# Optimization experiments

Measured on AMD Instinct MI355X. Metric: run time of the kernel, lower is better.

Reference implementation:

```python
import jax, jax.numpy as jnp
import numpy as np

B, SQ, SK, D_MODEL, H, D = 2, 2048, 2048, 1024, 16, 64


def setup_inputs() -> dict:
    key = jax.random.key(0)
    ks = jax.random.split(key, 10)
    s = 1.0 / np.sqrt(D_MODEL)
    return {
        "x": jax.random.normal(ks[0], (B, SK, D_MODEL), jnp.float32),
        "x2": jax.random.normal(ks[1], (B, SQ, D_MODEL), jnp.float32),
        "Wq": jax.random.normal(ks[2], (H, D_MODEL, D), jnp.float32) * s,
        "bq": jax.random.normal(ks[3], (H, D), jnp.float32) * s,
        "Wk": jax.random.normal(ks[4], (H, D_MODEL, D), jnp.float32) * s,
        "bk": jax.random.normal(ks[5], (H, D), jnp.float32) * s,
        "Wv": jax.random.normal(ks[6], (H, D_MODEL, D), jnp.float32) * s,
        "bv": jax.random.normal(ks[7], (H, D), jnp.float32) * s,
        "Wo": jax.random.normal(ks[8], (D_MODEL, D_MODEL), jnp.float32) * s,
        "bo": jax.random.normal(ks[9], (D_MODEL,), jnp.float32) * s,
    }


def reference(x, x2, Wq, bq, Wk, bk, Wv, bv, Wo, bo):
    # Batched per-head projections (fuses the Python per-head loop).
    # q: [B, H, SQ, D]; k,v: [B, H, SK, D]
    q = jnp.einsum("bsm,hmd->bhsd", x2, Wq) + bq[None, :, None, :]
    k = jnp.einsum("bsm,hmd->bhsd", x, Wk) + bk[None, :, None, :]
    v = jnp.einsum("bsm,hmd->bhsd", x, Wv) + bv[None, :, None, :]
    scale = 1.0 / jnp.sqrt(jnp.asarray(D, q.dtype))
    scores = jnp.einsum("bhqd,bhkd->bhqk", q, k) * scale  # [B,H,SQ,SK]
    attn = jax.nn.softmax(scores, axis=-1)
    o = jnp.einsum("bhqk,bhkd->bhqd", attn, v)  # [B,H,SQ,D]
    # concat heads along feature dim (head-major order matches torch.cat)
    o = o.transpose(0, 2, 1, 3).reshape(B, SQ, H * D)
    # final projection; dropout is identity in eval mode
    return o @ Wo.T + bo
```

## Files before the change

### kernel.cpp

```cpp
#include <hip/hip_runtime.h>
#include <math.h>

#define B_   2
#define SQ_  2048
#define SK_  2048
#define DM_  1024
#define H_   16
#define D_   64

typedef __attribute__((ext_vector_type(8))) short bf16x8;
typedef __attribute__((ext_vector_type(4))) float f32x4;
typedef unsigned int u32;

__device__ __forceinline__ short f2bf(float f) {
    union { float f; unsigned u; } v; v.f = f;
    unsigned r = v.u + 0x7FFFu + ((v.u >> 16) & 1u);
    return (short)(r >> 16);
}
__device__ __forceinline__ u32 pk2bf(float x, float y) {
    union { float f; u32 u; } a, b; a.f = x; b.f = y;
    return ((a.u + 0x8000u) >> 16) | ((b.u + 0x8000u) & 0xFFFF0000u);
}

__device__ __forceinline__ void gll16(const void* g, void* l) {
    __builtin_amdgcn_global_load_lds(
        (const __attribute__((address_space(1))) u32*)g,
        (__attribute__((address_space(3))) u32*)l, 16, 0, 0);
}

__global__ __launch_bounds__(256) void prep_kernel(
    const float* __restrict__ Wq, const float* __restrict__ Wk,
    const float* __restrict__ Wv, const float* __restrict__ Wo,
    const float* __restrict__ x,  const float* __restrict__ x2,
    short* __restrict__ WqT, short* __restrict__ WkT,
    short* __restrict__ WvT, short* __restrict__ Wob,
    short* __restrict__ xb,  short* __restrict__ x2b)
{
    const int t = threadIdx.x;
    const int z = blockIdx.z;
    if (z >= 3) {
        const float* src = (z == 3) ? Wo : (z == 4) ? x : x2;
        short* dst       = (z == 3) ? Wob : (z == 4) ? xb : x2b;
        int nloop = (z == 3) ? 4 : 16;
        int bid = blockIdx.y * 16 + blockIdx.x;
        #pragma unroll 4
        for (int j = 0; j < nloop; j++) {
            int i = bid * (nloop * 256) + j * 256 + t;
            float4 v = ((const float4*)src)[i];
            short4 s;
            s.x = f2bf(v.x); s.y = f2bf(v.y); s.z = f2bf(v.z); s.w = f2bf(v.w);
            ((short4*)dst)[i] = s;
        }
        return;
    }
    const float* W = (z == 0) ? Wq : (z == 1) ? Wk : Wv;
    short* WT      = (z == 0) ? WqT : (z == 1) ? WkT : WvT;
    const int h  = blockIdx.y;
    const int m0 = blockIdx.x * 64;
    __shared__ short Ls[64][68];

    #pragma unroll
    for (int it = 0; it < 4; it++) {
        int lin = it * 256 + t;
        int m = lin >> 4, d4 = lin & 15;
        float4 v = *(const float4*)&W[((long)h * DM_ + m0 + m) * D_ + d4 * 4];
        short4 s;
        s.x = f2bf(v.x); s.y = f2bf(v.y); s.z = f2bf(v.z); s.w = f2bf(v.w);
        *(short4*)&Ls[m][d4 * 4] = s;
    }
    __syncthreads();
    #pragma unroll
    for (int it = 0; it < 2; it++) {
        int d = (t >> 3) + it * 32, scol = t & 7;
        bf16x8 vv;
        #pragma unroll
        for (int j = 0; j < 8; j++) vv[j] = Ls[scol * 8 + j][d];
        *(bf16x8*)&WT[((long)h * 64 + d) * DM_ + m0 + scol * 8] = vv;
    }
}

template <int MODE>
__device__ __forceinline__ void gemm_core(
    const short* __restrict__ A, const short* __restrict__ Bw,
    const float* __restrict__ bias, void* __restrict__ outp,
    int r0, int n0, float oscale)
{
    __shared__ short As[128 * 64];
    __shared__ short Bs[128 * 64];

    const int t    = threadIdx.x;
    const int w    = t >> 6;
    const int ln   = t & 63;
    const int l15  = ln & 15;
    const int quad = ln >> 4;
    const int wr   = w >> 1;
    const int wc   = w & 1;

    f32x4 acc[4][4];
    #pragma unroll
    for (int i = 0; i < 4; i++)
        #pragma unroll
        for (int j = 0; j < 4; j++) acc[i][j] = (f32x4){0.f, 0.f, 0.f, 0.f};

    const int srow = ln >> 3;
    const int sc   = (ln & 7) ^ srow;
    const int rsw  = l15 & 7;

    for (int k0 = 0; k0 < 1024; k0 += 64) {
        __syncthreads();
        #pragma unroll
        for (int j = 0; j < 4; j++) {
            int q   = w * 4 + j;
            int row = q * 8 + srow;
            gll16(A  + ((long)(r0 + row) << 10) + k0 + sc * 8, As + q * 512);
            gll16(Bw + ((long)(n0 + row) << 10) + k0 + sc * 8, Bs + q * 512);
        }
        __syncthreads();
        #pragma unroll
        for (int kh = 0; kh < 2; kh++) {
            bf16x8 af[4], bfr[4];
            #pragma unroll
            for (int i = 0; i < 4; i++) {
                int ra = wr * 64 + i * 16 + l15;
                int rb = wc * 64 + i * 16 + l15;
                int pc = ((kh * 4 + quad) ^ rsw) * 8;
                af[i]  = *(const bf16x8*)&As[ra * 64 + pc];
                bfr[i] = *(const bf16x8*)&Bs[rb * 64 + pc];
            }
            #pragma unroll
            for (int i = 0; i < 4; i++)
                #pragma unroll
                for (int j = 0; j < 4; j++)
                    acc[i][j] = __builtin_amdgcn_mfma_f32_16x16x32_bf16(
                        af[i], bfr[j], acc[i][j], 0, 0, 0);
        }
    }

    #pragma unroll
    for (int j = 0; j < 4; j++) {
        int col = n0 + wc * 64 + j * 16 + l15;
        float bv = bias[col];
        if (MODE == 2) {
            int hh = col >> 6, dd = col & 63;
            #pragma unroll
            for (int i = 0; i < 4; i++) {
                int rowb = r0 + wr * 64 + i * 16 + quad * 4;
                int bb = rowb >> 11, ss = rowb & 2047;
                short4 sv;
                sv.x = f2bf(acc[i][j][0] + bv);
                sv.y = f2bf(acc[i][j][1] + bv);
                sv.z = f2bf(acc[i][j][2] + bv);
                sv.w = f2bf(acc[i][j][3] + bv);
                *(short4*)&((short*)outp)[
                    ((long)(((bb << 4) + hh) * 64 + dd) << 11) + ss] = sv;
            }
        } else {
            #pragma unroll
            for (int i = 0; i < 4; i++) {
                int rowb = r0 + wr * 64 + i * 16 + quad * 4;
                #pragma unroll
                for (int r = 0; r < 4; r++) {
                    float v = (acc[i][j][r] + bv) * oscale;
                    if (MODE == 0)
                        ((short*)outp)[(long)(rowb + r) * 1024 + col] = f2bf(v);
                    else
                        ((float*)outp)[(long)(rowb + r) * 1024 + col] = v;
                }
            }
        }
    }
}

#define QSCALE 0.180336880977f

__global__ __launch_bounds__(256) void gemm_qkv_kernel(
    const short* __restrict__ x2b, const short* __restrict__ xb,
    const short* __restrict__ WqT, const short* __restrict__ WkT,
    const short* __restrict__ WvT,
    const float* __restrict__ bq, const float* __restrict__ bk,
    const float* __restrict__ bv,
    short* __restrict__ Qb, short* __restrict__ Kb, short* __restrict__ VT)
{
    const int z = blockIdx.z;
    if (z == 0) {
        gemm_core<0>(x2b, WqT, bq, Qb, blockIdx.x * 128, blockIdx.y * 128, QSCALE);
    } else if (z == 1) {
        gemm_core<0>(xb, WkT, bk, Kb, blockIdx.x * 128, blockIdx.y * 128, 1.0f);
    } else {
        gemm_core<2>(xb, WvT, bv, VT, blockIdx.x * 128, blockIdx.y * 128, 1.0f);
    }
}

__global__ __launch_bounds__(256) void gemm_out_kernel(
    const short* __restrict__ A, const short* __restrict__ Bw,
    const float* __restrict__ bias, float* __restrict__ outp)
{
    __shared__ short As[64 * 64];
    __shared__ short Bs[128 * 64];

    const int r0   = blockIdx.x * 64;
    const int n0   = blockIdx.y * 128;
    const int t    = threadIdx.x;
    const int w    = t >> 6;
    const int ln   = t & 63;
    const int l15  = ln & 15;
    const int quad = ln >> 4;
    const int wr   = w >> 1;
    const int wc   = w & 1;

    f32x4 acc[2][4];
    #pragma unroll
    for (int i = 0; i < 2; i++)
        #pragma unroll
        for (int j = 0; j < 4; j++) acc[i][j] = (f32x4){0.f, 0.f, 0.f, 0.f};

    const int srow = ln >> 3;
    const int sc   = (ln & 7) ^ srow;
    const int rsw  = l15 & 7;

    for (int k0 = 0; k0 < 1024; k0 += 64) {
        __syncthreads();
        #pragma unroll
        for (int j = 0; j < 6; j++) {
            int q = w * 6 + j;
            if (q < 8) {
                int row = q * 8 + srow;
                gll16(A + ((long)(r0 + row) << 10) + k0 + sc * 8, As + q * 512);
            } else {
                int qb = q - 8;
                int row = qb * 8 + srow;
                gll16(Bw + ((long)(n0 + row) << 10) + k0 + sc * 8, Bs + qb * 512);
            }
        }
        __syncthreads();
        #pragma unroll
        for (int kh = 0; kh < 2; kh++) {
            int pc = ((kh * 4 + quad) ^ rsw) * 8;
            bf16x8 af[2], bfr[4];
            #pragma unroll
            for (int i = 0; i < 2; i++)
                af[i] = *(const bf16x8*)&As[(wr * 32 + i * 16 + l15) * 64 + pc];
            #pragma unroll
            for (int j = 0; j < 4; j++)
                bfr[j] = *(const bf16x8*)&Bs[(wc * 64 + j * 16 + l15) * 64 + pc];
            #pragma unroll
            for (int i = 0; i < 2; i++)
                #pragma unroll
                for (int j = 0; j < 4; j++)
                    acc[i][j] = __builtin_amdgcn_mfma_f32_16x16x32_bf16(
                        af[i], bfr[j], acc[i][j], 0, 0, 0);
        }
    }

    #pragma unroll
    for (int j = 0; j < 4; j++) {
        int col = n0 + wc * 64 + j * 16 + l15;
        float bv = bias[col];
        #pragma unroll
        for (int i = 0; i < 2; i++) {
            int rowb = r0 + wr * 32 + i * 16 + quad * 4;
            #pragma unroll
            for (int r = 0; r < 4; r++)
                outp[(long)(rowb + r) * 1024 + col] = acc[i][j][r] + bv;
        }
    }
}

__global__ __launch_bounds__(256) void flash_kernel(
    const short* __restrict__ Q, const short* __restrict__ K,
    const short* __restrict__ VT, short* __restrict__ O)
{
    const int t    = threadIdx.x;
    const int wave = t >> 6;
    const int ln   = t & 63;
    const int l15  = ln & 15;
    const int quad = ln >> 4;
    const int bh = blockIdx.y;
    const int b  = bh >> 4;
    const int h  = bh & 15;
    const int q0 = blockIdx.x * 64;
    const int wq = q0 + wave * 16;

    __shared__ short Ks[64 * 64];
    __shared__ short Vs[64 * 64];
    __shared__ short Ps[4][16 * 72];

    const int srow = ln >> 3;
    const int sc   = (ln & 7) ^ srow;
    const int rsw  = l15 & 7;

    bf16x8 aQ0, aQ1;
    {
        const short* Qp = Q + ((long)(b * SQ_ + wq + l15)) * 1024 + h * 64 + quad * 8;
        aQ0 = *(const bf16x8*)(Qp);
        aQ1 = *(const bf16x8*)(Qp + 32);
    }

    bf16x8 ones;
    #pragma unroll
    for (int j = 0; j < 8; j++) ones[j] = (short)0x3F80;

    f32x4 o_acc[4];
    #pragma unroll
    for (int i = 0; i < 4; i++) o_acc[i] = (f32x4){0.f, 0.f, 0.f, 0.f};
    f32x4 l_acc = (f32x4){0.f, 0.f, 0.f, 0.f};

    const short* Kbase = K  + ((long)b * SK_) * 1024 + h * 64;
    const short* Vbase = VT + (long)bh * D_ * SK_;

    for (int k0 = 0; k0 < SK_; k0 += 64) {
        __syncthreads();
        #pragma unroll
        for (int it = 0; it < 2; ++it) {
            int qq  = wave * 2 + it;
            int row = qq * 8 + srow;
            gll16(Kbase + (long)(k0 + row) * 1024 + sc * 8, Ks + qq * 512);
            gll16(Vbase + (long)row * 2048 + k0 + sc * 8,   Vs + qq * 512);
        }
        __syncthreads();

        f32x4 st[4];
        #pragma unroll
        for (int kt = 0; kt < 4; kt++) {
            const short* kr = &Ks[(kt * 16 + l15) * 64];
            bf16x8 ka0 = *(const bf16x8*)&kr[((quad    ) ^ rsw) * 8];
            bf16x8 ka1 = *(const bf16x8*)&kr[((quad + 4) ^ rsw) * 8];
            f32x4 z = (f32x4){0.f, 0.f, 0.f, 0.f};
            z = __builtin_amdgcn_mfma_f32_16x16x32_bf16(ka0, aQ0, z, 0, 0, 0);
            z = __builtin_amdgcn_mfma_f32_16x16x32_bf16(ka1, aQ1, z, 0, 0, 0);
            st[kt] = z;
        }

        short* pr = &Ps[wave][l15 * 72];
        #pragma unroll
        for (int kt = 0; kt < 4; kt++) {
            float p0 = __builtin_amdgcn_exp2f(st[kt][0]);
            float p1 = __builtin_amdgcn_exp2f(st[kt][1]);
            float p2 = __builtin_amdgcn_exp2f(st[kt][2]);
            float p3 = __builtin_amdgcn_exp2f(st[kt][3]);
            uint2 wv; wv.x = pk2bf(p0, p1); wv.y = pk2bf(p2, p3);
            *(uint2*)&pr[(4 * kt + quad) * 4] = wv;
        }

        bf16x8 aP0 = *(const bf16x8*)&pr[quad * 8];
        bf16x8 aP1 = *(const bf16x8*)&pr[(quad + 4) * 8];
        l_acc = __builtin_amdgcn_mfma_f32_16x16x32_bf16(aP0, ones, l_acc, 0, 0, 0);
        l_acc = __builtin_amdgcn_mfma_f32_16x16x32_bf16(aP1, ones, l_acc, 0, 0, 0);
        #pragma unroll
        for (int dt = 0; dt < 4; dt++) {
            const short* vr = &Vs[(dt * 16 + l15) * 64];
            bf16x8 bv0 = *(const bf16x8*)&vr[((quad    ) ^ rsw) * 8];
            bf16x8 bv1 = *(const bf16x8*)&vr[((quad + 4) ^ rsw) * 8];
            o_acc[dt] = __builtin_amdgcn_mfma_f32_16x16x32_bf16(aP0, bv0, o_acc[dt], 0, 0, 0);
            o_acc[dt] = __builtin_amdgcn_mfma_f32_16x16x32_bf16(aP1, bv1, o_acc[dt], 0, 0, 0);
        }
    }

    #pragma unroll
    for (int r = 0; r < 4; r++) {
        float inv = 1.0f / l_acc[r];
        long row = (long)b * SQ_ + wq + quad * 4 + r;
        short* Op = O + row * 1024 + h * 64 + l15;
        #pragma unroll
        for (int dt = 0; dt < 4; dt++)
            Op[dt * 16] = f2bf(o_acc[dt][r] * inv);
    }
}

extern "C" void kernel_launch(void* const* d_in, const int* in_sizes, int n_in,
                              void* d_out, int out_size, void* d_ws, size_t ws_size,
                              hipStream_t stream) {
    const float* x  = (const float*)d_in[0];
    const float* x2 = (const float*)d_in[1];
    const float* Wq = (const float*)d_in[2];
    const float* bq = (const float*)d_in[3];
    const float* Wk = (const float*)d_in[4];
    const float* bk = (const float*)d_in[5];
    const float* Wv = (const float*)d_in[6];
    const float* bv = (const float*)d_in[7];
    const float* Wo = (const float*)d_in[8];
    const float* bo = (const float*)d_in[9];
    float* out = (float*)d_out;

    const size_t nAct = (size_t)B_ * SK_ * DM_;
    const size_t nW   = (size_t)DM_ * DM_;
    short* bufA = (short*)d_ws;
    short* bufB = bufA + nAct;
    short* Qb   = bufB + nAct;
    short* Kb   = Qb + nAct;
    short* VTws = Kb + nAct;
    short* WqT  = VTws + nAct;
    short* WkT  = WqT + nW;
    short* WvT  = WkT + nW;
    short* Wob  = WvT + nW;

    prep_kernel<<<dim3(16, 16, 6), 256, 0, stream>>>(
        Wq, Wk, Wv, Wo, x, x2, WqT, WkT, WvT, Wob, bufA, bufB);

    gemm_qkv_kernel<<<dim3(32, 8, 3), 256, 0, stream>>>(
        bufB, bufA, WqT, WkT, WvT, bq, bk, bv, Qb, Kb, VTws);

    flash_kernel<<<dim3(32, 32), 256, 0, stream>>>(Qb, Kb, VTws, bufB);
    gemm_out_kernel<<<dim3(64, 8), 256, 0, stream>>>(bufB, Wob, bo, out);
}
```

Baseline: 223.3 us.

## Double-buffer K/V tiles, keep P in registers, and double queries per wave

The flash kernel now double-buffers the K and V shared-memory tiles, prefetching the next tile while computing on the current one, which removes one barrier per iteration. P no longer round-trips through shared memory; V^T is written with a permuted sequence order so the MFMA output layout can feed the P·V MFMA directly from registers. Each wave now handles 32 query rows instead of 16, which halves the grid and reuses each K/V fragment across two query groups. This costs more registers and fewer blocks, which may lower occupancy.

```diff
diff --git a/kernel.cpp b/kernel.cpp
--- a/kernel.cpp
+++ b/kernel.cpp
@@ -146,13 +146,15 @@
             for (int i = 0; i < 4; i++) {
                 int rowb = r0 + wr * 64 + i * 16 + quad * 4;
                 int bb = rowb >> 11, ss = rowb & 2047;
+                int sl = ss & 63;
+                int sp = (ss & ~63) | (sl & 35) | ((sl & 12) << 1) | ((sl & 16) >> 2);
                 short4 sv;
                 sv.x = f2bf(acc[i][j][0] + bv);
                 sv.y = f2bf(acc[i][j][1] + bv);
                 sv.z = f2bf(acc[i][j][2] + bv);
                 sv.w = f2bf(acc[i][j][3] + bv);
                 *(short4*)&((short*)outp)[
-                    ((long)(((bb << 4) + hh) * 64 + dd) << 11) + ss] = sv;
+                    ((long)(((bb << 4) + hh) * 64 + dd) << 11) + sp] = sv;
             }
         } else {
             #pragma unroll
@@ -278,92 +280,119 @@
     const int bh = blockIdx.y;
     const int b  = bh >> 4;
     const int h  = bh & 15;
-    const int q0 = blockIdx.x * 64;
-    const int wq = q0 + wave * 16;
-
-    __shared__ short Ks[64 * 64];
-    __shared__ short Vs[64 * 64];
-    __shared__ short Ps[4][16 * 72];
+    const int q0 = blockIdx.x * 128;
+    const int wq = q0 + wave * 32;
+
+    __shared__ short Ks[2][64 * 64];
+    __shared__ short Vs[2][64 * 64];
 
     const int srow = ln >> 3;
     const int sc   = (ln & 7) ^ srow;
     const int rsw  = l15 & 7;
 
-    bf16x8 aQ0, aQ1;
-    {
-        const short* Qp = Q + ((long)(b * SQ_ + wq + l15)) * 1024 + h * 64 + quad * 8;
-        aQ0 = *(const bf16x8*)(Qp);
-        aQ1 = *(const bf16x8*)(Qp + 32);
+    bf16x8 aQ0[2], aQ1[2];
+    #pragma unroll
+    for (int qg = 0; qg < 2; qg++) {
+        const short* Qp = Q + ((long)(b * SQ_ + wq + qg * 16 + l15)) * 1024
+                            + h * 64 + quad * 8;
+        aQ0[qg] = *(const bf16x8*)(Qp);
+        aQ1[qg] = *(const bf16x8*)(Qp + 32);
     }
 
     bf16x8 ones;
     #pragma unroll
     for (int j = 0; j < 8; j++) ones[j] = (short)0x3F80;
 
-    f32x4 o_acc[4];
-    #pragma unroll
-    for (int i = 0; i < 4; i++) o_acc[i] = (f32x4){0.f, 0.f, 0.f, 0.f};
-    f32x4 l_acc = (f32x4){0.f, 0.f, 0.f, 0.f};
+    f32x4 o_acc[2][4];
+    f32x4 l_acc[2];
+    #pragma unroll
+    for (int qg = 0; qg < 2; qg++) {
+        l_acc[qg] = (f32x4){0.f, 0.f, 0.f, 0.f};
+        #pragma unroll
+        for (int i = 0; i < 4; i++) o_acc[qg][i] = (f32x4){0.f, 0.f, 0.f, 0.f};
+    }
 
     const short* Kbase = K  + ((long)b * SK_) * 1024 + h * 64;
     const short* Vbase = VT + (long)bh * D_ * SK_;
-
+    const int qqa = wave * 2, qqb = wave * 2 + 1;
+    const int rowa = qqa * 8 + srow, rowb_ = qqb * 8 + srow;
+
+    gll16(Kbase + (long)rowa  * 1024 + sc * 8, &Ks[0][qqa * 512]);
+    gll16(Vbase + (long)rowa  * 2048 + sc * 8, &Vs[0][qqa * 512]);
+    gll16(Kbase + (long)rowb_ * 1024 + sc * 8, &Ks[0][qqb * 512]);
+    gll16(Vbase + (long)rowb_ * 2048 + sc * 8, &Vs[0][qqb * 512]);
+
+    int cur = 0;
     for (int k0 = 0; k0 < SK_; k0 += 64) {
         __syncthreads();
-        #pragma unroll
-        for (int it = 0; it < 2; ++it) {
-            int qq  = wave * 2 + it;
-            int row = qq * 8 + srow;
-            gll16(Kbase + (long)(k0 + row) * 1024 + sc * 8, Ks + qq * 512);
-            gll16(Vbase + (long)row * 2048 + k0 + sc * 8,   Vs + qq * 512);
-        }
-        __syncthreads();
-
-        f32x4 st[4];
+        if (k0 + 64 < SK_) {
+            int nx = cur ^ 1;
+            gll16(Kbase + (long)(k0 + 64 + rowa)  * 1024 + sc * 8, &Ks[nx][qqa * 512]);
+            gll16(Vbase + (long)rowa  * 2048 + (k0 + 64) + sc * 8, &Vs[nx][qqa * 512]);
+            gll16(Kbase + (long)(k0 + 64 + rowb_) * 1024 + sc * 8, &Ks[nx][qqb * 512]);
+            gll16(Vbase + (long)rowb_ * 2048 + (k0 + 64) + sc * 8, &Vs[nx][qqb * 512]);
+        }
+        const short* Kst = Ks[cur];
+        const short* Vst = Vs[cur];
+
+        u32 pw[2][8];
         #pragma unroll
         for (int kt = 0; kt < 4; kt++) {
-            const short* kr = &Ks[(kt * 16 + l15) * 64];
+            const short* kr = &Kst[(kt * 16 + l15) * 64];
             bf16x8 ka0 = *(const bf16x8*)&kr[((quad    ) ^ rsw) * 8];
             bf16x8 ka1 = *(const bf16x8*)&kr[((quad + 4) ^ rsw) * 8];
-            f32x4 z = (f32x4){0.f, 0.f, 0.f, 0.f};
-            z = __builtin_amdgcn_mfma_f32_16x16x32_bf16(ka0, aQ0, z, 0, 0, 0);
-            z = __builtin_amdgcn_mfma_f32_16x16x32_bf16(ka1, aQ1, z, 0, 0, 0);
-            st[kt] = z;
-        }
-
-        short* pr = &Ps[wave][l15 * 72];
-        #pragma unroll
-        for (int kt = 0; kt < 4; kt++) {
-            float p0 = __builtin_amdgcn_exp2f(st[kt][0]);
-            float p1 = __builtin_amdgcn_exp2f(st[kt][1]);
-            float p2 = __builtin_amdgcn_exp2f(st[kt][2]);
-            float p3 = __builtin_amdgcn_exp2f(st[kt][3]);
-            uint2 wv; wv.x = pk2bf(p0, p1); wv.y = pk2bf(p2, p3);
-            *(uint2*)&pr[(4 * kt + quad) * 4] = wv;
-        }
-
-        bf16x8 aP0 = *(const bf16x8*)&pr[quad * 8];
-        bf16x8 aP1 = *(const bf16x8*)&pr[(quad + 4) * 8];
-        l_acc = __builtin_amdgcn_mfma_f32_16x16x32_bf16(aP0, ones, l_acc, 0, 0, 0);
-        l_acc = __builtin_amdgcn_mfma_f32_16x16x32_bf16(aP1, ones, l_acc, 0, 0, 0);
+            #pragma unroll
+            for (int qg = 0; qg < 2; qg++) {
+                f32x4 z = (f32x4){0.f, 0.f, 0.f, 0.f};
+                z = __builtin_amdgcn_mfma_f32_16x16x32_bf16(ka0, aQ0[qg], z, 0, 0, 0);
+                z = __builtin_amdgcn_mfma_f32_16x16x32_bf16(ka1, aQ1[qg], z, 0, 0, 0);
+                float p0 = __builtin_amdgcn_exp2f(z[0]);
+                float p1 = __builtin_amdgcn_exp2f(z[1]);
+                float p2 = __builtin_amdgcn_exp2f(z[2]);
+                float p3 = __builtin_amdgcn_exp2f(z[3]);
+                pw[qg][kt * 2    ] = pk2bf(p0, p1);
+                pw[qg][kt * 2 + 1] = pk2bf(p2, p3);
+            }
+        }
+
+        bf16x8 aP0[2], aP1[2];
+        #pragma unroll
+        for (int qg = 0; qg < 2; qg++) {
+            union { bf16x8 v; u32 w[4]; } u0, u1;
+            u0.w[0] = pw[qg][0]; u0.w[1] = pw[qg][1];
+            u0.w[2] = pw[qg][2]; u0.w[3] = pw[qg][3];
+            u1.w[0] = pw[qg][4]; u1.w[1] = pw[qg][5];
+            u1.w[2] = pw[qg][6]; u1.w[3] = pw[qg][7];
+            aP0[qg] = u0.v; aP1[qg] = u1.v;
+            l_acc[qg] = __builtin_amdgcn_mfma_f32_16x16x32_bf16(aP0[qg], ones, l_acc[qg], 0, 0, 0);
+            l_acc[qg] = __builtin_amdgcn_mfma_f32_16x16x32_bf16(aP1[qg], ones, l_acc[qg], 0, 0, 0);
+        }
+
         #pragma unroll
         for (int dt = 0; dt < 4; dt++) {
-            const short* vr = &Vs[(dt * 16 + l15) * 64];
+            const short* vr = &Vst[(dt * 16 + l15) * 64];
             bf16x8 bv0 = *(const bf16x8*)&vr[((quad    ) ^ rsw) * 8];
             bf16x8 bv1 = *(const bf16x8*)&vr[((quad + 4) ^ rsw) * 8];
-            o_acc[dt] = __builtin_amdgcn_mfma_f32_16x16x32_bf16(aP0, bv0, o_acc[dt], 0, 0, 0);
-            o_acc[dt] = __builtin_amdgcn_mfma_f32_16x16x32_bf16(aP1, bv1, o_acc[dt], 0, 0, 0);
-        }
-    }
-
-    #pragma unroll
-    for (int r = 0; r < 4; r++) {
-        float inv = 1.0f / l_acc[r];
-        long row = (long)b * SQ_ + wq + quad * 4 + r;
-        short* Op = O + row * 1024 + h * 64 + l15;
-        #pragma unroll
-        for (int dt = 0; dt < 4; dt++)
-            Op[dt * 16] = f2bf(o_acc[dt][r] * inv);
+            #pragma unroll
+            for (int qg = 0; qg < 2; qg++) {
+                o_acc[qg][dt] = __builtin_amdgcn_mfma_f32_16x16x32_bf16(aP0[qg], bv0, o_acc[qg][dt], 0, 0, 0);
+                o_acc[qg][dt] = __builtin_amdgcn_mfma_f32_16x16x32_bf16(aP1[qg], bv1, o_acc[qg][dt], 0, 0, 0);
+            }
+        }
+        cur ^= 1;
+    }
+
+    #pragma unroll
+    for (int qg = 0; qg < 2; qg++) {
+        #pragma unroll
+        for (int r = 0; r < 4; r++) {
+            float inv = 1.0f / l_acc[qg][r];
+            long row = (long)b * SQ_ + wq + qg * 16 + quad * 4 + r;
+            short* Op = O + row * 1024 + h * 64 + l15;
+            #pragma unroll
+            for (int dt = 0; dt < 4; dt++)
+                Op[dt * 16] = f2bf(o_acc[qg][dt][r] * inv);
+        }
     }
 }
 
@@ -400,6 +429,6 @@
     gemm_qkv_kernel<<<dim3(32, 8, 3), 256, 0, stream>>>(
         bufB, bufA, WqT, WkT, WvT, bq, bk, bv, Qb, Kb, VTws);
 
-    flash_kernel<<<dim3(32, 32), 256, 0, stream>>>(Qb, Kb, VTws, bufB);
+    flash_kernel<<<dim3(16, 32), 256, 0, stream>>>(Qb, Kb, VTws, bufB);
     gemm_out_kernel<<<dim3(64, 8), 256, 0, stream>>>(bufB, Wob, bo, out);
 }
```

New measurement: 209.6 us. 1.07x faster.
